# Kernel tuning notes

Measured on AMD Instinct MI355X. Metric: run time of the kernel, lower is better.

The kernel has to match this reference:

```python
import jax, jax.numpy as jnp
import numpy as np

N_USERS = 100_000
N_ITEMS = 50_000
N_NODES = N_USERS + N_ITEMS   # 150000
NNZ_URM = 2_000_000           # user-item interactions
N_EDGES = 2 * NNZ_URM         # symmetric bipartite adjacency
EMB = 64
HOPS = 3
BATCH = 16384
EPS = 1e-6


def setup_inputs() -> dict:
    key = jax.random.key(0)
    k_u, k_i, k_e, k_ub, k_ib = jax.random.split(key, 5)
    # random implicit-feedback interactions (binary URM)
    u = jax.random.randint(k_u, (NNZ_URM,), 0, N_USERS, dtype=jnp.int32)
    it = jax.random.randint(k_i, (NNZ_URM,), 0, N_ITEMS, dtype=jnp.int32) + N_USERS
    # A = [[0, URM], [URM^T, 0]] in COO form
    edge_row = jnp.concatenate([u, it])
    edge_col = jnp.concatenate([it, u])
    # symmetric normalization: D^-1/2 A D^-1/2 (URM values are 1.0)
    deg = jax.ops.segment_sum(jnp.ones((N_EDGES,), jnp.float32), edge_row,
                              num_segments=N_NODES)
    d_inv = 1.0 / (jnp.sqrt(deg) + EPS)
    edge_val = d_inv[edge_row] * d_inv[edge_col]
    # E_0 ~ Normal(0, 0.1) as in torch.nn.init.normal_(std=0.1)
    E_0 = 0.1 * jax.random.normal(k_e, (N_NODES, EMB), dtype=jnp.float32)
    user_batch = jax.random.randint(k_ub, (BATCH,), 0, N_USERS, dtype=jnp.int32)
    item_batch = jax.random.randint(k_ib, (BATCH,), 0, N_ITEMS, dtype=jnp.int32)
    return {"E_0": E_0, "edge_val": edge_val, "edge_row": edge_row,
            "edge_col": edge_col, "user_batch": user_batch,
            "item_batch": item_batch, "K": HOPS}


def reference(E_0, edge_val, edge_row, edge_col, user_batch, item_batch, K):
    def spmm(E):
        # sparse.mm(A_tilde, E): gather rows of E by col, scale, scatter-add by row
        return jax.ops.segment_sum(edge_val[:, None] * E[edge_col], edge_row,
                                   num_segments=N_NODES)

    E_i = E_0
    E_sum = E_0
    for _ in range(K):
        E_i = spmm(E_i)
        E_sum = E_sum + E_i
    E_final = E_sum / (K + 1)
    user_factors = E_final[:N_USERS]
    item_factors = E_final[N_USERS:]
    # einsum('bk,bk->b')
    prediction = jnp.sum(user_factors[user_batch] * item_factors[item_batch],
                         axis=-1)
    return prediction
```

## Files before the change

### kernel.cpp

```cpp
#include <hip/hip_runtime.h>

#define N_USERS 100000
#define N_ITEMS 50000
#define N_NODES 150000
#define NEDGES  4000000
#define EMB     64
#define BATCH   16384

#define RSHIFT  9
#define RPB     512
#define NBKT    ((N_NODES + RPB - 1) / RPB)
#define BCAP    24576

#define PC_BS   1024
#define PC_CH   16384
#define PC_EPT  (PC_CH / PC_BS)
#define PC_NWG  ((NEDGES + PC_CH - 1) / PC_CH)


__device__ __forceinline__ unsigned short f2b(float f) {
    unsigned u = __float_as_uint(f);
    return (unsigned short)((u + 0x7FFFu + ((u >> 16) & 1u)) >> 16);
}
__device__ __forceinline__ float b2f_lo(unsigned v) { return __uint_as_float(v << 16); }
__device__ __forceinline__ float b2f_hi(unsigned v) { return __uint_as_float(v & 0xFFFF0000u); }

__device__ __forceinline__ void acc8(float* a, uint4 v) {
    a[0] += b2f_lo(v.x); a[1] += b2f_hi(v.x);
    a[2] += b2f_lo(v.y); a[3] += b2f_hi(v.y);
    a[4] += b2f_lo(v.z); a[5] += b2f_hi(v.z);
    a[6] += b2f_lo(v.w); a[7] += b2f_hi(v.w);
}


__global__ void k_zero(int* __restrict__ bcursor) {
    int i = blockIdx.x * blockDim.x + threadIdx.x;
    if (i < NBKT) bcursor[i] = 0;
}

__global__ __launch_bounds__(PC_BS) void k_partC(const int* __restrict__ erow,
                                                 const int* __restrict__ ecol,
                                                 int* __restrict__ bcursor,
                                                 unsigned* __restrict__ tmp) {
    __shared__ int cnt[NBKT];
    __shared__ int base_[NBKT];
    const int t = threadIdx.x;
    for (int i = t; i < NBKT; i += PC_BS) cnt[i] = 0;
    __syncthreads();
    const int e0 = blockIdx.x * PC_CH;
    int rr[PC_EPT], cc[PC_EPT];
#pragma unroll
    for (int k = 0; k < PC_EPT; ++k) {
        int e = e0 + t + k * PC_BS;
        if (e < NEDGES) {
            rr[k] = erow[e];
            cc[k] = ecol[e];
            atomicAdd(&cnt[rr[k] >> RSHIFT], 1);
        } else rr[k] = -1;
    }
    __syncthreads();
    for (int i = t; i < NBKT; i += PC_BS) {
        base_[i] = cnt[i] ? atomicAdd(&bcursor[i], cnt[i]) : 0;
        cnt[i] = 0;
    }
    __syncthreads();
#pragma unroll
    for (int k = 0; k < PC_EPT; ++k) {
        if (rr[k] >= 0) {
            int b = rr[k] >> RSHIFT;
            int pos = base_[b] + atomicAdd(&cnt[b], 1);
            if (pos < BCAP)
                tmp[(size_t)b * BCAP + pos] =
                    ((unsigned)(rr[k] & (RPB - 1)) << 18) | (unsigned)cc[k];
        }
    }
}

__global__ __launch_bounds__(512) void k_bscan(const int* __restrict__ bcursor,
                                               int* __restrict__ bbase,
                                               int* __restrict__ rowptr) {
    __shared__ int s[512];
    const int t = threadIdx.x;
    int v = 0;
    if (t < NBKT) { v = bcursor[t]; if (v > BCAP) v = BCAP; }
    s[t] = v;
    __syncthreads();
    for (int off = 1; off < 512; off <<= 1) {
        int u = (t >= off) ? s[t - off] : 0;
        __syncthreads();
        s[t] += u;
        __syncthreads();
    }
    if (t < NBKT) bbase[t] = s[t] - v;
    if (t == 511) { bbase[NBKT] = s[511]; rowptr[N_NODES] = s[511]; }
}

__global__ __launch_bounds__(512) void k_rows_place(const unsigned* __restrict__ tmp,
                                                    const int* __restrict__ bcursor,
                                                    const int* __restrict__ bbase,
                                                    int* __restrict__ rowptr,
                                                    float* __restrict__ dinv,
                                                    float* __restrict__ s2,
                                                    float* __restrict__ srt,
                                                    int* __restrict__ csrc) {
    __shared__ int rc[RPB];
    __shared__ int pre[RPB];
    const int b = blockIdx.x;
    const int t = threadIdx.x;
    rc[t] = 0;
    __syncthreads();
    int n = bcursor[b]; if (n > BCAP) n = BCAP;
    const unsigned* tp = tmp + (size_t)b * BCAP;
    for (int i = t; i < n; i += 512) atomicAdd(&rc[tp[i] >> 18], 1);
    __syncthreads();
    int my = rc[t];
    pre[t] = my;
    __syncthreads();
    for (int off = 1; off < 512; off <<= 1) {
        int u = (t >= off) ? pre[t - off] : 0;
        __syncthreads();
        pre[t] += u;
        __syncthreads();
    }
    int ex   = pre[t] - my;
    int base = bbase[b];
    int r = b * RPB + t;
    if (r < N_NODES) {
        float sr = sqrtf((float)my) + 1e-6f;
        float dv = 1.0f / sr;
        rowptr[r] = base + ex;
        dinv[r] = dv;
        s2[r]   = dv * dv;
        srt[r]  = sr;
    }
    __syncthreads();
    rc[t] = base + ex;
    __syncthreads();
    for (int i = t; i < n; i += 512) {
        unsigned pk = tp[i];
        int slot = atomicAdd(&rc[pk >> 18], 1);
        csrc[slot] = (int)(pk & 0x3FFFFu);
    }
}

__global__ void k_cast(const float* __restrict__ E0, const float* __restrict__ dinv,
                       unsigned short* __restrict__ F0) {
    int i = blockIdx.x * blockDim.x + threadIdx.x;
    const int total = N_NODES * EMB / 4;
    if (i >= total) return;
    float dv = dinv[i >> 4];
    float4 v = ((const float4*)E0)[i];
    ushort4 o;
    o.x = f2b(dv * v.x); o.y = f2b(dv * v.y);
    o.z = f2b(dv * v.z); o.w = f2b(dv * v.w);
    ((ushort4*)F0)[i] = o;
}


__device__ __forceinline__ void spmm_row(const unsigned short* __restrict__ Fin,
                                         unsigned short* __restrict__ Fout,
                                         const int* __restrict__ cols,
                                         int beg, int end, int g, int lane, float s) {
    float A[8] = {0,0,0,0,0,0,0,0};
    float B[8] = {0,0,0,0,0,0,0,0};
    int j = beg;
    int nscal = (4 - (j & 3)) & 3;
    for (int k = 0; k < nscal && j < end; ++k, ++j) {
        uint4 v = ((const uint4*)(Fin + (size_t)cols[j] * EMB))[lane];
        acc8(A, v);
    }
    for (; j + 8 <= end; j += 8) {
        int4 c0 = *(const int4*)(cols + j);
        int4 c1 = *(const int4*)(cols + j + 4);
        uint4 v0 = ((const uint4*)(Fin + (size_t)c0.x * EMB))[lane];
        uint4 v1 = ((const uint4*)(Fin + (size_t)c0.y * EMB))[lane];
        uint4 v2 = ((const uint4*)(Fin + (size_t)c0.z * EMB))[lane];
        uint4 v3 = ((const uint4*)(Fin + (size_t)c0.w * EMB))[lane];
        uint4 v4 = ((const uint4*)(Fin + (size_t)c1.x * EMB))[lane];
        uint4 v5 = ((const uint4*)(Fin + (size_t)c1.y * EMB))[lane];
        uint4 v6 = ((const uint4*)(Fin + (size_t)c1.z * EMB))[lane];
        uint4 v7 = ((const uint4*)(Fin + (size_t)c1.w * EMB))[lane];
        acc8(A, v0); acc8(B, v1); acc8(A, v2); acc8(B, v3);
        acc8(A, v4); acc8(B, v5); acc8(A, v6); acc8(B, v7);
    }
    for (; j + 4 <= end; j += 4) {
        int4 c = *(const int4*)(cols + j);
        uint4 v0 = ((const uint4*)(Fin + (size_t)c.x * EMB))[lane];
        uint4 v1 = ((const uint4*)(Fin + (size_t)c.y * EMB))[lane];
        uint4 v2 = ((const uint4*)(Fin + (size_t)c.z * EMB))[lane];
        uint4 v3 = ((const uint4*)(Fin + (size_t)c.w * EMB))[lane];
        acc8(A, v0); acc8(B, v1); acc8(A, v2); acc8(B, v3);
    }
    for (; j < end; ++j) {
        uint4 v = ((const uint4*)(Fin + (size_t)cols[j] * EMB))[lane];
        acc8(A, v);
    }
    unsigned o0 = ((unsigned)f2b(s * (A[1] + B[1])) << 16) | f2b(s * (A[0] + B[0]));
    unsigned o1 = ((unsigned)f2b(s * (A[3] + B[3])) << 16) | f2b(s * (A[2] + B[2]));
    unsigned o2 = ((unsigned)f2b(s * (A[5] + B[5])) << 16) | f2b(s * (A[4] + B[4]));
    unsigned o3 = ((unsigned)f2b(s * (A[7] + B[7])) << 16) | f2b(s * (A[6] + B[6]));
    ((uint4*)(Fout + (size_t)g * EMB))[lane] = make_uint4(o0, o1, o2, o3);
}

__global__ __launch_bounds__(256) void k_spmm(const unsigned short* __restrict__ Fin,
                                              unsigned short* __restrict__ Fout,
                                              const int* __restrict__ rowptr,
                                              const int* __restrict__ cols,
                                              const float* __restrict__ s2) {
    int g    = (blockIdx.x * blockDim.x + threadIdx.x) >> 3;
    int lane = threadIdx.x & 7;
    if (g >= N_NODES) return;
    spmm_row(Fin, Fout, cols, rowptr[g], rowptr[g + 1], g, lane, s2[g]);
}

__global__ __launch_bounds__(256) void k_spmm3(const unsigned short* __restrict__ Fin,
                                               unsigned short* __restrict__ Fout,
                                               const int* __restrict__ rowptr,
                                               const int* __restrict__ cols,
                                               const float* __restrict__ s2,
                                               const int* __restrict__ ub,
                                               const int* __restrict__ ib) {
    int gi   = (blockIdx.x * blockDim.x + threadIdx.x) >> 3;
    int lane = threadIdx.x & 7;
    if (gi >= 2 * BATCH) return;
    int g = (gi < BATCH) ? ub[gi] : (N_USERS + ib[gi - BATCH]);
    spmm_row(Fin, Fout, cols, rowptr[g], rowptr[g + 1], g, lane, s2[g]);
}


__global__ void k_gather_init(const float* __restrict__ E0, const int* __restrict__ ub,
                              const int* __restrict__ ib, float* __restrict__ U,
                              float* __restrict__ I) {
    int g    = (blockIdx.x * blockDim.x + threadIdx.x) >> 4;
    int lane = threadIdx.x & 15;
    if (g >= 2 * BATCH) return;
    if (g < BATCH) {
        int r = ub[g];
        ((float4*)(U + (size_t)g * EMB))[lane] =
            ((const float4*)(E0 + (size_t)r * EMB))[lane];
    } else {
        int bq = g - BATCH;
        int r = N_USERS + ib[bq];
        ((float4*)(I + (size_t)bq * EMB))[lane] =
            ((const float4*)(E0 + (size_t)r * EMB))[lane];
    }
}

__global__ void k_gather_acc(const unsigned short* __restrict__ F,
                             const float* __restrict__ srt,
                             const int* __restrict__ ub, const int* __restrict__ ib,
                             float* __restrict__ U, float* __restrict__ I) {
    int g    = (blockIdx.x * blockDim.x + threadIdx.x) >> 4;
    int lane = threadIdx.x & 15;
    if (g >= 2 * BATCH) return;
    int r, bq;
    float* dstbuf;
    if (g < BATCH) { r = ub[g]; bq = g; dstbuf = U; }
    else { bq = g - BATCH; r = N_USERS + ib[bq]; dstbuf = I; }
    float sr = srt[r];
    uint2 v = ((const uint2*)(F + (size_t)r * EMB))[lane];
    float4* dst = (float4*)(dstbuf + (size_t)bq * EMB) + lane;
    float4 a = *dst;
    a.x = fmaf(sr, b2f_lo(v.x), a.x); a.y = fmaf(sr, b2f_hi(v.x), a.y);
    a.z = fmaf(sr, b2f_lo(v.y), a.z); a.w = fmaf(sr, b2f_hi(v.y), a.w);
    *dst = a;
}


__global__ void k_finish(const unsigned short* __restrict__ F3,
                         const float* __restrict__ srt,
                         const int* __restrict__ ub, const int* __restrict__ ib,
                         const float* __restrict__ U, const float* __restrict__ I,
                         float* __restrict__ out) {
    int q    = (blockIdx.x * blockDim.x + threadIdx.x) >> 4;
    int lane = threadIdx.x & 15;
    if (q >= BATCH) return;
    int u  = ub[q];
    int iv = N_USERS + ib[q];
    float su = srt[u], si = srt[iv];
    float4 a = ((const float4*)(U + (size_t)q * EMB))[lane];
    float4 b = ((const float4*)(I + (size_t)q * EMB))[lane];
    uint2 vu = ((const uint2*)(F3 + (size_t)u * EMB))[lane];
    uint2 vi = ((const uint2*)(F3 + (size_t)iv * EMB))[lane];
    a.x = fmaf(su, b2f_lo(vu.x), a.x); a.y = fmaf(su, b2f_hi(vu.x), a.y);
    a.z = fmaf(su, b2f_lo(vu.y), a.z); a.w = fmaf(su, b2f_hi(vu.y), a.w);
    b.x = fmaf(si, b2f_lo(vi.x), b.x); b.y = fmaf(si, b2f_hi(vi.x), b.y);
    b.z = fmaf(si, b2f_lo(vi.y), b.z); b.w = fmaf(si, b2f_hi(vi.y), b.w);
    float p = a.x * b.x + a.y * b.y + a.z * b.z + a.w * b.w;
    for (int m = 1; m < 16; m <<= 1) p += __shfl_xor(p, m, 64);
    if (lane == 0) out[q] = p * (1.0f / 16.0f);
}


static inline char* align16(char* p) {
    return (char*)(((uintptr_t)p + 15) & ~(uintptr_t)15);
}

extern "C" void kernel_launch(void* const* d_in, const int* in_sizes, int n_in,
                              void* d_out, int out_size, void* d_ws, size_t ws_size,
                              hipStream_t stream) {
    const float* E0   = (const float*)d_in[0];
    const int*   erow = (const int*)d_in[2];
    const int*   ecol = (const int*)d_in[3];
    const int*   ub   = (const int*)d_in[4];
    const int*   ib   = (const int*)d_in[5];
    float* pred = (float*)d_out;

    char* p = (char*)d_ws;
    unsigned short* F0  = (unsigned short*)p; p = align16(p + (size_t)N_NODES * EMB * 2);
    unsigned short* Abf = (unsigned short*)p; p = align16(p + (size_t)N_NODES * EMB * 2);
    unsigned short* Bbf = (unsigned short*)p; p = align16(p + (size_t)N_NODES * EMB * 2);
    float* U       = (float*)p;    p = align16(p + (size_t)BATCH * EMB * 4);
    float* I       = (float*)p;    p = align16(p + (size_t)BATCH * EMB * 4);
    int*   bcursor = (int*)p;      p = align16(p + (size_t)NBKT * 4);
    int*   bbase   = (int*)p;      p = align16(p + (size_t)(NBKT + 1) * 4);
    int*   rowptr  = (int*)p;      p = align16(p + (size_t)(N_NODES + 1) * 4);
    float* dinv    = (float*)p;    p = align16(p + (size_t)N_NODES * 4);
    float* s2      = (float*)p;    p = align16(p + (size_t)N_NODES * 4);
    float* srt     = (float*)p;    p = align16(p + (size_t)N_NODES * 4);
    int*   csrc    = (int*)p;      p = align16(p + (size_t)NEDGES * 4);
    unsigned* tmp  = (unsigned*)p; p = align16(p + (size_t)NBKT * BCAP * 4);

    const int BS = 256;
    k_zero<<<(NBKT + BS - 1) / BS, BS, 0, stream>>>(bcursor);
    k_partC<<<PC_NWG, PC_BS, 0, stream>>>(erow, ecol, bcursor, tmp);
    k_bscan<<<1, 512, 0, stream>>>(bcursor, bbase, rowptr);
    k_rows_place<<<NBKT, 512, 0, stream>>>(tmp, bcursor, bbase, rowptr, dinv, s2, srt, csrc);
    k_cast<<<(N_NODES * EMB / 4 + BS - 1) / BS, BS, 0, stream>>>(E0, dinv, F0);

    k_gather_init<<<(2 * BATCH * 16 + BS - 1) / BS, BS, 0, stream>>>(E0, ub, ib, U, I);

    const int spmm_grid = (N_NODES * 8 + BS - 1) / BS;
    const int acc_grid  = (2 * BATCH * 16 + BS - 1) / BS;

    k_spmm<<<spmm_grid, BS, 0, stream>>>(F0, Abf, rowptr, csrc, s2);
    k_gather_acc<<<acc_grid, BS, 0, stream>>>(Abf, srt, ub, ib, U, I);
    k_spmm<<<spmm_grid, BS, 0, stream>>>(Abf, Bbf, rowptr, csrc, s2);
    k_gather_acc<<<acc_grid, BS, 0, stream>>>(Bbf, srt, ub, ib, U, I);
    k_spmm3<<<(2 * BATCH * 8 + BS - 1) / BS, BS, 0, stream>>>(Bbf, Abf, rowptr, csrc,
                                                              s2, ub, ib);
    k_finish<<<(BATCH * 16 + BS - 1) / BS, BS, 0, stream>>>(Abf, srt, ub, ib, U, I, pred);
}
```

Baseline: 247.5 us.

## Sort rows by degree and use persistent atomic-chunk scheduling in SpMM

Builds a degree histogram during CSR construction, scans it, and scatters row ids into a permutation grouped by degree. The full SpMM hops then run as a persistent kernel of 2048 blocks that grab 32-row chunks through a global atomic counter and process rows in degree order. The aim is to balance load across wavefronts so rows of similar length run together, reducing divergence and tail imbalance. In exchange it adds two setup kernels, an atomic plus two block barriers per chunk, and output writes that are no longer spatially coherent.

New measurement: 336.4 us. 1.36x slower.

```diff
diff --git a/kernel.cpp b/kernel.cpp
--- a/kernel.cpp
+++ b/kernel.cpp
@@ -17,6 +17,9 @@
 #define PC_EPT  (PC_CH / PC_BS)
 #define PC_NWG  ((NEDGES + PC_CH - 1) / PC_CH)
 
+#define CHROWS  32
+#define NCHUNK  ((N_NODES + CHROWS - 1) / CHROWS)
+
 
 __device__ __forceinline__ unsigned short f2b(float f) {
     unsigned u = __float_as_uint(f);
@@ -33,9 +36,10 @@
 }
 
 
-__global__ void k_zero(int* __restrict__ bcursor) {
+__global__ void k_zero(int* __restrict__ bcursor, int* __restrict__ ghist) {
     int i = blockIdx.x * blockDim.x + threadIdx.x;
     if (i < NBKT) bcursor[i] = 0;
+    if (i < 256) ghist[i] = 0;
 }
 
 __global__ __launch_bounds__(PC_BS) void k_partC(const int* __restrict__ erow,
@@ -102,12 +106,15 @@
                                                     float* __restrict__ dinv,
                                                     float* __restrict__ s2,
                                                     float* __restrict__ srt,
-                                                    int* __restrict__ csrc) {
+                                                    int* __restrict__ csrc,
+                                                    int* __restrict__ ghist) {
     __shared__ int rc[RPB];
     __shared__ int pre[RPB];
+    __shared__ int dh[256];
     const int b = blockIdx.x;
     const int t = threadIdx.x;
     rc[t] = 0;
+    if (t < 256) dh[t] = 0;
     __syncthreads();
     int n = bcursor[b]; if (n > BCAP) n = BCAP;
     const unsigned* tp = tmp + (size_t)b * BCAP;
@@ -132,14 +139,63 @@
         dinv[r] = dv;
         s2[r]   = dv * dv;
         srt[r]  = sr;
-    }
-    __syncthreads();
+        int bin = my > 255 ? 255 : my;
+        atomicAdd(&dh[bin], 1);
+    }
+    __syncthreads();
+    if (t < 256 && dh[t]) atomicAdd(&ghist[t], dh[t]);
     rc[t] = base + ex;
     __syncthreads();
     for (int i = t; i < n; i += 512) {
         unsigned pk = tp[i];
         int slot = atomicAdd(&rc[pk >> 18], 1);
         csrc[slot] = (int)(pk & 0x3FFFFu);
+    }
+}
+
+__global__ __launch_bounds__(256) void k_dscan(const int* __restrict__ ghist,
+                                               int* __restrict__ gcur,
+                                               int* __restrict__ ctrs) {
+    __shared__ int s[256];
+    const int t = threadIdx.x;
+    int v = ghist[t];
+    s[t] = v;
+    __syncthreads();
+    for (int off = 1; off < 256; off <<= 1) {
+        int u = (t >= off) ? s[t - off] : 0;
+        __syncthreads();
+        s[t] += u;
+        __syncthreads();
+    }
+    gcur[t] = s[t] - v;
+    if (t < 8) ctrs[t] = 0;
+}
+
+__global__ __launch_bounds__(512) void k_permscat(const int* __restrict__ rowptr,
+                                                  int* __restrict__ gcur,
+                                                  int* __restrict__ perm) {
+    __shared__ int cnt[256];
+    __shared__ int base_[256];
+    const int b = blockIdx.x;
+    const int t = threadIdx.x;
+    if (t < 256) cnt[t] = 0;
+    __syncthreads();
+    int r = b * RPB + t;
+    int bin = -1;
+    if (r < N_NODES) {
+        int deg = rowptr[r + 1] - rowptr[r];
+        bin = deg > 255 ? 255 : deg;
+        atomicAdd(&cnt[bin], 1);
+    }
+    __syncthreads();
+    if (t < 256) {
+        base_[t] = cnt[t] ? atomicAdd(&gcur[t], cnt[t]) : 0;
+        cnt[t] = 0;
+    }
+    __syncthreads();
+    if (r < N_NODES) {
+        int pos = base_[bin] + atomicAdd(&cnt[bin], 1);
+        perm[pos] = r;
     }
 }
 
@@ -206,11 +262,24 @@
                                               unsigned short* __restrict__ Fout,
                                               const int* __restrict__ rowptr,
                                               const int* __restrict__ cols,
-                                              const float* __restrict__ s2) {
-    int g    = (blockIdx.x * blockDim.x + threadIdx.x) >> 3;
-    int lane = threadIdx.x & 7;
-    if (g >= N_NODES) return;
-    spmm_row(Fin, Fout, cols, rowptr[g], rowptr[g + 1], g, lane, s2[g]);
+                                              const float* __restrict__ s2,
+                                              const int* __restrict__ perm,
+                                              int* __restrict__ ctr) {
+    __shared__ int chnk;
+    const int lane = threadIdx.x & 7;
+    const int grp  = threadIdx.x >> 3;
+    for (;;) {
+        if (threadIdx.x == 0) chnk = atomicAdd(ctr, 1);
+        __syncthreads();
+        int c = chnk;
+        __syncthreads();
+        if (c >= NCHUNK) break;
+        int idx = c * CHROWS + grp;
+        if (idx < N_NODES) {
+            int g = perm[idx];
+            spmm_row(Fin, Fout, cols, rowptr[g], rowptr[g + 1], g, lane, s2[g]);
+        }
+    }
 }
 
 __global__ __launch_bounds__(256) void k_spmm3(const unsigned short* __restrict__ Fin,
@@ -318,24 +387,31 @@
     float* dinv    = (float*)p;    p = align16(p + (size_t)N_NODES * 4);
     float* s2      = (float*)p;    p = align16(p + (size_t)N_NODES * 4);
     float* srt     = (float*)p;    p = align16(p + (size_t)N_NODES * 4);
+    int*   ghist   = (int*)p;      p = align16(p + 256 * 4);
+    int*   gcur    = (int*)p;      p = align16(p + 256 * 4);
+    int*   ctrs    = (int*)p;      p = align16(p + 8 * 4);
+    int*   perm    = (int*)p;      p = align16(p + (size_t)N_NODES * 4);
     int*   csrc    = (int*)p;      p = align16(p + (size_t)NEDGES * 4);
     unsigned* tmp  = (unsigned*)p; p = align16(p + (size_t)NBKT * BCAP * 4);
 
     const int BS = 256;
-    k_zero<<<(NBKT + BS - 1) / BS, BS, 0, stream>>>(bcursor);
+    k_zero<<<(NBKT + BS - 1) / BS, BS, 0, stream>>>(bcursor, ghist);
     k_partC<<<PC_NWG, PC_BS, 0, stream>>>(erow, ecol, bcursor, tmp);
     k_bscan<<<1, 512, 0, stream>>>(bcursor, bbase, rowptr);
-    k_rows_place<<<NBKT, 512, 0, stream>>>(tmp, bcursor, bbase, rowptr, dinv, s2, srt, csrc);
+    k_rows_place<<<NBKT, 512, 0, stream>>>(tmp, bcursor, bbase, rowptr, dinv, s2, srt,
+                                           csrc, ghist);
+    k_dscan<<<1, 256, 0, stream>>>(ghist, gcur, ctrs);
+    k_permscat<<<NBKT, 512, 0, stream>>>(rowptr, gcur, perm);
     k_cast<<<(N_NODES * EMB / 4 + BS - 1) / BS, BS, 0, stream>>>(E0, dinv, F0);
 
     k_gather_init<<<(2 * BATCH * 16 + BS - 1) / BS, BS, 0, stream>>>(E0, ub, ib, U, I);
 
-    const int spmm_grid = (N_NODES * 8 + BS - 1) / BS;
-    const int acc_grid  = (2 * BATCH * 16 + BS - 1) / BS;
-
-    k_spmm<<<spmm_grid, BS, 0, stream>>>(F0, Abf, rowptr, csrc, s2);
+    const int acc_grid = (2 * BATCH * 16 + BS - 1) / BS;
+    const int spmm_blocks = 2048;
+
+    k_spmm<<<spmm_blocks, BS, 0, stream>>>(F0, Abf, rowptr, csrc, s2, perm, ctrs + 0);
     k_gather_acc<<<acc_grid, BS, 0, stream>>>(Abf, srt, ub, ib, U, I);
-    k_spmm<<<spmm_grid, BS, 0, stream>>>(Abf, Bbf, rowptr, csrc, s2);
+    k_spmm<<<spmm_blocks, BS, 0, stream>>>(Abf, Bbf, rowptr, csrc, s2, perm, ctrs + 1);
     k_gather_acc<<<acc_grid, BS, 0, stream>>>(Bbf, srt, ub, ib, U, I);
     k_spmm3<<<(2 * BATCH * 8 + BS - 1) / BS, BS, 0, stream>>>(Bbf, Abf, rowptr, csrc,
                                                               s2, ub, ib);
```
